# Optimization experiments

Hardware: AMD Instinct MI355X
Metric: run time of the kernel (lower is better)

The kernel has to match this reference:

```python
import jax, jax.numpy as jnp
import numpy as np

HEADS = 16
DIM_HEAD = 64
QUERY_DIM = 1024
INNER = HEADS * DIM_HEAD
SCALE = DIM_HEAD ** -0.5


def setup_inputs() -> dict:
    key = jax.random.key(0)
    ks = jax.random.split(key, 6)
    B, N, M = 2, 2048, 2048
    x = jax.random.normal(ks[0], (B, N, QUERY_DIM), dtype=jnp.float32)
    context = jax.random.normal(ks[1], (B, M, QUERY_DIM), dtype=jnp.float32)
    s = QUERY_DIM ** -0.5
    # weights stored [in, out] so y = x @ W matches torch Linear(x) with W = weight.T
    Wq = jax.random.normal(ks[2], (QUERY_DIM, INNER), dtype=jnp.float32) * s
    Wk = jax.random.normal(ks[3], (QUERY_DIM, INNER), dtype=jnp.float32) * s
    Wv = jax.random.normal(ks[4], (QUERY_DIM, INNER), dtype=jnp.float32) * s
    Wo = jax.random.normal(ks[5], (INNER, QUERY_DIM), dtype=jnp.float32) * (INNER ** -0.5)
    return {"x": x, "context": context, "Wq": Wq, "Wk": Wk, "Wv": Wv, "Wo": Wo}


def reference(x, context, Wq, Wk, Wv, Wo):
    B, N, _ = x.shape
    M = context.shape[1]
    # projections -> [b, n, h, d]
    q = (x @ Wq).reshape(B, N, HEADS, DIM_HEAD)
    k = (context @ Wk).reshape(B, M, HEADS, DIM_HEAD)
    v = (context @ Wv).reshape(B, M, HEADS, DIM_HEAD)
    sim = jnp.einsum('bihd,bjhd->bhij', q, k) * SCALE  # [b, h, n, m]
    attn = jax.nn.softmax(sim, axis=-1)
    out = jnp.einsum('bhij,bjhd->bihd', attn, v)  # [b, n, h, d]
    out = out.reshape(B, N, INNER)
    return out @ Wo
```

## Files before the change

### kernel.cpp

```cpp
#include <hip/hip_runtime.h>
#include <hip/hip_bf16.h>


typedef __attribute__((ext_vector_type(8))) __bf16    bf16x8;
typedef __attribute__((ext_vector_type(4))) __bf16    bf16x4;
typedef __attribute__((ext_vector_type(4))) float     f32x4;

#define B_    2
#define H_    16
#define N_    2048
#define M_    2048
#define D_    64
#define QD_   1024

#define QSCALE 0.18033688011112042f

__device__ __forceinline__ void gld16(const __bf16* g, __bf16* l) {
    __builtin_amdgcn_global_load_lds(
        (const __attribute__((address_space(1))) unsigned int*)(g),
        (__attribute__((address_space(3))) unsigned int*)(l), 16, 0, 0);
}

__global__ __launch_bounds__(256) void prep(const float* __restrict__ x,
                                            const float* __restrict__ ctx,
                                            const float* __restrict__ w0,
                                            const float* __restrict__ w1,
                                            const float* __restrict__ w2,
                                            const float* __restrict__ w3,
                                            __bf16* __restrict__ xb,
                                            __bf16* __restrict__ cb,
                                            __bf16* __restrict__ t0,
                                            __bf16* __restrict__ t1,
                                            __bf16* __restrict__ t2,
                                            __bf16* __restrict__ t3) {
    __shared__ float tile[64][65];
    const int z = blockIdx.z;
    if (z < 2) {
        const float* src = z ? ctx : x;
        __bf16*      dst = z ? cb  : xb;
        const size_t base = (size_t)(blockIdx.y * 16 + blockIdx.x) * 16384;
#pragma unroll
        for (int p = 0; p < 16; ++p) {
            size_t i = base + p * 1024 + threadIdx.x * 4;
            float4 v = *reinterpret_cast<const float4*>(src + i);
            bf16x4 o;
            o.x = (__bf16)v.x; o.y = (__bf16)v.y; o.z = (__bf16)v.z; o.w = (__bf16)v.w;
            *reinterpret_cast<bf16x4*>(dst + i) = o;
        }
        return;
    }
    const int w = z - 2;
    const float* in = (w == 0) ? w0 : (w == 1) ? w1 : (w == 2) ? w2 : w3;
    __bf16*     out = (w == 0) ? t0 : (w == 1) ? t1 : (w == 2) ? t2 : t3;
    const int i0 = blockIdx.x * 64;
    const int o0 = blockIdx.y * 64;
    const int t  = threadIdx.x;
    const int r  = t >> 4;
    const int c4 = (t & 15) * 4;
#pragma unroll
    for (int p = 0; p < 4; ++p) {
        int row = p * 16 + r;
        float4 v = *reinterpret_cast<const float4*>(in + (size_t)(i0 + row) * QD_ + o0 + c4);
        tile[row][c4 + 0] = v.x; tile[row][c4 + 1] = v.y;
        tile[row][c4 + 2] = v.z; tile[row][c4 + 3] = v.w;
    }
    __syncthreads();
#pragma unroll
    for (int p = 0; p < 4; ++p) {
        int orow = p * 16 + r;
        bf16x4 o;
        o.x = (__bf16)tile[c4 + 0][orow];
        o.y = (__bf16)tile[c4 + 1][orow];
        o.z = (__bf16)tile[c4 + 2][orow];
        o.w = (__bf16)tile[c4 + 3][orow];
        *reinterpret_cast<bf16x4*>(out + (size_t)(o0 + orow) * QD_ + i0 + c4) = o;
    }
}

__global__ __launch_bounds__(256) void gemm_qkv(const __bf16* __restrict__ xb,
                                                const __bf16* __restrict__ cb,
                                                const __bf16* __restrict__ Wtq,
                                                const __bf16* __restrict__ Wtk,
                                                const __bf16* __restrict__ Wtv,
                                                __bf16* __restrict__ Qb,
                                                __bf16* __restrict__ Kb,
                                                __bf16* __restrict__ Vt) {
    __shared__ __align__(16) __bf16 POOL[17408];
    __bf16* const Al0 = POOL;
    __bf16* const Al1 = POOL + 4096;
    __bf16* const Bl0 = POOL + 8192;
    __bf16* const Bl1 = POOL + 12288;

    const int z = blockIdx.z;
    const __bf16* A_  = (z == 0) ? xb : cb;
    const __bf16* Bt_ = (z == 0) ? Wtq : (z == 1) ? Wtk : Wtv;

    const int tid  = threadIdx.x;
    const int wid  = tid >> 6;
    const int lane = tid & 63;
    const int l15  = lane & 15;
    const int lg   = lane >> 4;
    const int wr   = wid >> 1;
    const int wc   = wid & 1;
    const int rowBase = blockIdx.x * 128;
    const int colBase = blockIdx.y * 128;
    const int srow = wid * 32 + (lane >> 2);
    const int sg   = ((lane & 3) ^ ((srow >> 1) & 3)) * 8;
    const __bf16* Ag  = A_  + (size_t)(rowBase + srow) * QD_ + sg;
    const __bf16* Ag2 = Ag  + (size_t)16 * QD_;
    const __bf16* Bg  = Bt_ + (size_t)(colBase + srow) * QD_ + sg;
    const __bf16* Bg2 = Bg  + (size_t)16 * QD_;
    const int sOff  = (wid * 32) * 32;
    const int sOff2 = sOff + 16 * 32;
    int aoff[4], boff[4];
#pragma unroll
    for (int m = 0; m < 4; ++m) {
        int ra = wr * 64 + m * 16 + l15;
        int rb = wc * 64 + m * 16 + l15;
        aoff[m] = ra * 32 + ((lg ^ ((ra >> 1) & 3)) * 8);
        boff[m] = rb * 32 + ((lg ^ ((rb >> 1) & 3)) * 8);
    }
    f32x4 acc[4][4] = {};

#define GCOMPUTE(AL, BL)                                                                       \
    {                                                                                          \
        bf16x8 a[4], b[4];                                                                     \
        _Pragma("unroll")                                                                      \
        for (int m = 0; m < 4; ++m)                                                            \
            a[m] = *reinterpret_cast<const bf16x8*>(&(AL)[aoff[m]]);                           \
        _Pragma("unroll")                                                                      \
        for (int n = 0; n < 4; ++n)                                                            \
            b[n] = *reinterpret_cast<const bf16x8*>(&(BL)[boff[n]]);                           \
        _Pragma("unroll")                                                                      \
        for (int m = 0; m < 4; ++m)                                                            \
            _Pragma("unroll")                                                                  \
            for (int n = 0; n < 4; ++n)                                                        \
                acc[m][n] = __builtin_amdgcn_mfma_f32_16x16x32_bf16(a[m], b[n], acc[m][n], 0, 0, 0); \
    }

    gld16(Ag,  Al0 + sOff);
    gld16(Ag2, Al0 + sOff2);
    gld16(Bg,  Bl0 + sOff);
    gld16(Bg2, Bl0 + sOff2);
    __syncthreads();
    for (int t = 0; t < 32; t += 2) {
        if (t + 1 < 32) {
            int kn = (t + 1) * 32;
            gld16(Ag + kn,  Al1 + sOff);
            gld16(Ag2 + kn, Al1 + sOff2);
            gld16(Bg + kn,  Bl1 + sOff);
            gld16(Bg2 + kn, Bl1 + sOff2);
        }
        GCOMPUTE(Al0, Bl0)
        __syncthreads();
        if (t + 2 < 32) {
            int kn = (t + 2) * 32;
            gld16(Ag + kn,  Al0 + sOff);
            gld16(Ag2 + kn, Al0 + sOff2);
            gld16(Bg + kn,  Bl0 + sOff);
            gld16(Bg2 + kn, Bl0 + sOff2);
        }
        GCOMPUTE(Al1, Bl1)
        __syncthreads();
    }
#undef GCOMPUTE

#pragma unroll
    for (int m = 0; m < 4; ++m)
#pragma unroll
        for (int n = 0; n < 4; ++n)
#pragma unroll
            for (int r = 0; r < 4; ++r) {
                float v = acc[m][n][r];
                if (z == 0) v *= QSCALE;
                int rl = wr * 64 + m * 16 + lg * 4 + r;
                int cl = wc * 64 + n * 16 + l15;
                if (z == 2) POOL[cl * 136 + rl] = (__bf16)v;
                else        POOL[rl * 136 + cl] = (__bf16)v;
            }
    __syncthreads();

    const int prow0 = tid >> 4;
    const int pcol  = (tid & 15) * 8;
#pragma unroll
    for (int s = 0; s < 8; ++s) {
        int row = s * 16 + prow0;
        bf16x8 vv = *reinterpret_cast<const bf16x8*>(&POOL[row * 136 + pcol]);
        if (z == 2) {
            int cc = colBase + row, rr = rowBase + pcol;
            int b_ = rr >> 11, mm = rr & 2047, hh = cc >> 6, dd = cc & 63;
            *reinterpret_cast<bf16x8*>(&Vt[((size_t)(b_ * H_ + hh) * D_ + dd) * M_ + mm]) = vv;
        } else {
            int rr = rowBase + row, cc = colBase + pcol;
            int b_ = rr >> 11, nn = rr & 2047, hh = cc >> 6, dd = cc & 63;
            __bf16* dst = (z == 0) ? Qb : Kb;
            *reinterpret_cast<bf16x8*>(&dst[((size_t)(b_ * H_ + hh) * N_ + nn) * D_ + dd]) = vv;
        }
    }
}

__global__ __launch_bounds__(256) void gemm_out(const __bf16* __restrict__ AO,
                                                const __bf16* __restrict__ Wto,
                                                float* __restrict__ out) {
    __shared__ __align__(16) __bf16 POOL[17408];
    __bf16* const Al0 = POOL;
    __bf16* const Al1 = POOL + 4096;
    __bf16* const Bl0 = POOL + 8192;
    __bf16* const Bl1 = POOL + 10240;

    const int tid  = threadIdx.x;
    const int wid  = tid >> 6;
    const int lane = tid & 63;
    const int l15  = lane & 15;
    const int lg   = lane >> 4;
    const int wr   = wid >> 1;
    const int wc   = wid & 1;
    const int rowBase = blockIdx.x * 128;
    const int colBase = blockIdx.y * 64;
    const int srowA = wid * 32 + (lane >> 2);
    const int srowB = wid * 16 + (lane >> 2);
    const int sgA   = ((lane & 3) ^ ((srowA >> 1) & 3)) * 8;
    const int sgB   = ((lane & 3) ^ ((srowB >> 1) & 3)) * 8;
    const __bf16* Ag  = AO  + (size_t)(rowBase + srowA) * QD_ + sgA;
    const __bf16* Ag2 = Ag  + (size_t)16 * QD_;
    const __bf16* Bg  = Wto + (size_t)(colBase + srowB) * QD_ + sgB;
    const int sOffA  = (wid * 32) * 32;
    const int sOffA2 = sOffA + 16 * 32;
    const int sOffB  = (wid * 16) * 32;
    int aoff[4], boff[2];
#pragma unroll
    for (int m = 0; m < 4; ++m) {
        int ra = wr * 64 + m * 16 + l15;
        aoff[m] = ra * 32 + ((lg ^ ((ra >> 1) & 3)) * 8);
    }
#pragma unroll
    for (int n = 0; n < 2; ++n) {
        int rb = wc * 32 + n * 16 + l15;
        boff[n] = rb * 32 + ((lg ^ ((rb >> 1) & 3)) * 8);
    }
    f32x4 acc[4][2] = {};

#define GCOMPUTE2(AL, BL)                                                                      \
    {                                                                                          \
        bf16x8 a[4], b[2];                                                                     \
        _Pragma("unroll")                                                                      \
        for (int m = 0; m < 4; ++m)                                                            \
            a[m] = *reinterpret_cast<const bf16x8*>(&(AL)[aoff[m]]);                           \
        _Pragma("unroll")                                                                      \
        for (int n = 0; n < 2; ++n)                                                            \
            b[n] = *reinterpret_cast<const bf16x8*>(&(BL)[boff[n]]);                           \
        _Pragma("unroll")                                                                      \
        for (int m = 0; m < 4; ++m)                                                            \
            _Pragma("unroll")                                                                  \
            for (int n = 0; n < 2; ++n)                                                        \
                acc[m][n] = __builtin_amdgcn_mfma_f32_16x16x32_bf16(a[m], b[n], acc[m][n], 0, 0, 0); \
    }

    gld16(Ag,  Al0 + sOffA);
    gld16(Ag2, Al0 + sOffA2);
    gld16(Bg,  Bl0 + sOffB);
    __syncthreads();
    for (int t = 0; t < 32; t += 2) {
        if (t + 1 < 32) {
            int kn = (t + 1) * 32;
            gld16(Ag + kn,  Al1 + sOffA);
            gld16(Ag2 + kn, Al1 + sOffA2);
            gld16(Bg + kn,  Bl1 + sOffB);
        }
        GCOMPUTE2(Al0, Bl0)
        __syncthreads();
        if (t + 2 < 32) {
            int kn = (t + 2) * 32;
            gld16(Ag + kn,  Al0 + sOffA);
            gld16(Ag2 + kn, Al0 + sOffA2);
            gld16(Bg + kn,  Bl0 + sOffB);
        }
        GCOMPUTE2(Al1, Bl1)
        __syncthreads();
    }
#undef GCOMPUTE2

    float* FP = reinterpret_cast<float*>(POOL);
#pragma unroll
    for (int m = 0; m < 4; ++m)
#pragma unroll
        for (int n = 0; n < 2; ++n)
#pragma unroll
            for (int r = 0; r < 4; ++r) {
                int rl = wr * 64 + m * 16 + lg * 4 + r;
                int cl = wc * 32 + n * 16 + l15;
                FP[rl * 68 + cl] = acc[m][n][r];
            }
    __syncthreads();
    const int prow0 = tid >> 4;
    const int pcol4 = (tid & 15) * 4;
#pragma unroll
    for (int s = 0; s < 8; ++s) {
        int row = s * 16 + prow0;
        float4 vv = *reinterpret_cast<const float4*>(&FP[row * 68 + pcol4]);
        *reinterpret_cast<float4*>(&out[(size_t)(rowBase + row) * QD_ + colBase + pcol4]) = vv;
    }
}

__global__ __launch_bounds__(512, 4) void attn_kernel(const __bf16* __restrict__ Q,
                                                      const __bf16* __restrict__ K,
                                                      const __bf16* __restrict__ Vt,
                                                      __bf16* __restrict__ AO) {
    __shared__ __align__(16) __bf16 POOL[32768];

    const int logical = (blockIdx.x & 7) * 64 + (blockIdx.x >> 3);
    const int qt   = logical & 15;
    const int bh   = logical >> 4;
    const int b    = bh >> 4;
    const int h    = bh & 15;
    const int wid  = threadIdx.x >> 6;
    const int grp  = wid >> 2;
    const int wl   = wid & 3;
    const int lane = threadIdx.x & 63;
    const int l15  = lane & 15;
    const int lg   = lane >> 4;
    const int qbase = qt * 128 + wl * 32;
    const int kv0   = grp << 10;

    const __bf16* Qp = Q  + ((size_t)bh * N_ + qbase) * D_;
    const __bf16* Kp = K  + (size_t)bh * M_ * D_;
    const __bf16* Vp = Vt + (size_t)bh * D_ * M_;

    const int srow = (wl << 4) + (lane >> 3);
    const int scol = (lane & 7) << 3;
    const int sk0  = (lane >> 3) & 3;
    const int sk1  = sk0 | 4;
    const int sv   = lane >> 3;
    const int kc0  = scol ^ (sk0 << 3);
    const int kc1  = scol ^ (sk1 << 3);
    const int vc   = scol ^ (sv  << 3);

    __bf16* const K0 = POOL + (grp * 2 + 0) * 4096;
    __bf16* const K1 = POOL + (grp * 2 + 1) * 4096;
    __bf16* const V0 = POOL + 16384 + (grp * 2 + 0) * 4096;
    __bf16* const V1 = POOL + 16384 + (grp * 2 + 1) * 4096;
    __bf16* const k0d = K0 + wl * 1024;
    __bf16* const k1d = K1 + wl * 1024;
    __bf16* const v0d = V0 + wl * 1024;
    __bf16* const v1d = V1 + wl * 1024;

#define STAGE(KD, VD, KV)                                                      \
    gld16(Kp + (size_t)((KV) + srow)     * D_ + kc0, (KD));                    \
    gld16(Kp + (size_t)((KV) + srow + 8) * D_ + kc1, (KD) + 512);              \
    gld16(Vp + (size_t)(srow)     * M_ + (KV) + vc,  (VD));                    \
    gld16(Vp + (size_t)(srow + 8) * M_ + (KV) + vc,  (VD) + 512);

    const int rm0 = ((l15 >> 2) * 8) + (l15 & 3);
    const int skq = (l15 & 3) | (((l15 >> 2) & 1) << 2);
    const int svq = l15 & 7;
    const int ak00 = rm0 * 64 + (( 0 + lg * 8) ^ (skq << 3));
    const int ak01 = rm0 * 64 + ((32 + lg * 8) ^ (skq << 3));
    const int ak10 = ak00 + 256;
    const int ak11 = ak01 + 256;
    const int av0 = l15 * 64 + (( 0 + lg * 8) ^ (svq << 3));
    const int av1 = l15 * 64 + ((32 + lg * 8) ^ (svq << 3));

    bf16x8 qf00 = *reinterpret_cast<const bf16x8*>(Qp + (size_t)(l15)      * D_ +      lg * 8);
    bf16x8 qf01 = *reinterpret_cast<const bf16x8*>(Qp + (size_t)(l15)      * D_ + 32 + lg * 8);
    bf16x8 qf10 = *reinterpret_cast<const bf16x8*>(Qp + (size_t)(16 + l15) * D_ +      lg * 8);
    bf16x8 qf11 = *reinterpret_cast<const bf16x8*>(Qp + (size_t)(16 + l15) * D_ + 32 + lg * 8);

    bf16x8 onesf;
#pragma unroll
    for (int j = 0; j < 8; ++j) onesf[j] = (__bf16)1.0f;

    f32x4 o00 = {}, o01 = {}, o10 = {}, o11 = {};
    f32x4 o20 = {}, o21 = {}, o30 = {}, o31 = {};
    f32x4 ors0 = {}, ors1 = {};

#define COMPUTE(KB, VB, KOFF, AV)                                                               \
    {                                                                                           \
        bf16x8 k00 = *reinterpret_cast<const bf16x8*>((KB) + ak00 + (KOFF));                    \
        bf16x8 k01 = *reinterpret_cast<const bf16x8*>((KB) + ak01 + (KOFF));                    \
        bf16x8 k10 = *reinterpret_cast<const bf16x8*>((KB) + ak10 + (KOFF));                    \
        bf16x8 k11 = *reinterpret_cast<const bf16x8*>((KB) + ak11 + (KOFF));                    \
        bf16x8 v0  = *reinterpret_cast<const bf16x8*>((VB) + (AV));                             \
        bf16x8 v1  = *reinterpret_cast<const bf16x8*>((VB) + (AV) + 1024);                      \
        bf16x8 v2  = *reinterpret_cast<const bf16x8*>((VB) + (AV) + 2048);                      \
        bf16x8 v3  = *reinterpret_cast<const bf16x8*>((VB) + (AV) + 3072);                      \
        f32x4 s00 = {}, s01 = {}, s10 = {}, s11 = {};                                           \
        __builtin_amdgcn_s_setprio(1);                                                          \
        s00 = __builtin_amdgcn_mfma_f32_16x16x32_bf16(k00, qf00, s00, 0, 0, 0);                 \
        s00 = __builtin_amdgcn_mfma_f32_16x16x32_bf16(k01, qf01, s00, 0, 0, 0);                 \
        s01 = __builtin_amdgcn_mfma_f32_16x16x32_bf16(k00, qf10, s01, 0, 0, 0);                 \
        s01 = __builtin_amdgcn_mfma_f32_16x16x32_bf16(k01, qf11, s01, 0, 0, 0);                 \
        s10 = __builtin_amdgcn_mfma_f32_16x16x32_bf16(k10, qf00, s10, 0, 0, 0);                 \
        s10 = __builtin_amdgcn_mfma_f32_16x16x32_bf16(k11, qf01, s10, 0, 0, 0);                 \
        s11 = __builtin_amdgcn_mfma_f32_16x16x32_bf16(k10, qf10, s11, 0, 0, 0);                 \
        s11 = __builtin_amdgcn_mfma_f32_16x16x32_bf16(k11, qf11, s11, 0, 0, 0);                 \
        __builtin_amdgcn_s_setprio(0);                                                          \
        bf16x8 pf0, pf1;                                                                        \
        pf0[0] = (__bf16)__builtin_amdgcn_exp2f(s00[0]);                                        \
        pf0[1] = (__bf16)__builtin_amdgcn_exp2f(s00[1]);                                        \
        pf0[2] = (__bf16)__builtin_amdgcn_exp2f(s00[2]);                                        \
        pf0[3] = (__bf16)__builtin_amdgcn_exp2f(s00[3]);                                        \
        pf0[4] = (__bf16)__builtin_amdgcn_exp2f(s10[0]);                                        \
        pf0[5] = (__bf16)__builtin_amdgcn_exp2f(s10[1]);                                        \
        pf0[6] = (__bf16)__builtin_amdgcn_exp2f(s10[2]);                                        \
        pf0[7] = (__bf16)__builtin_amdgcn_exp2f(s10[3]);                                        \
        pf1[0] = (__bf16)__builtin_amdgcn_exp2f(s01[0]);                                        \
        pf1[1] = (__bf16)__builtin_amdgcn_exp2f(s01[1]);                                        \
        pf1[2] = (__bf16)__builtin_amdgcn_exp2f(s01[2]);                                        \
        pf1[3] = (__bf16)__builtin_amdgcn_exp2f(s01[3]);                                        \
        pf1[4] = (__bf16)__builtin_amdgcn_exp2f(s11[0]);                                        \
        pf1[5] = (__bf16)__builtin_amdgcn_exp2f(s11[1]);                                        \
        pf1[6] = (__bf16)__builtin_amdgcn_exp2f(s11[2]);                                        \
        pf1[7] = (__bf16)__builtin_amdgcn_exp2f(s11[3]);                                        \
        __builtin_amdgcn_s_setprio(1);                                                          \
        ors0 = __builtin_amdgcn_mfma_f32_16x16x32_bf16(pf0, onesf, ors0, 0, 0, 0);              \
        ors1 = __builtin_amdgcn_mfma_f32_16x16x32_bf16(pf1, onesf, ors1, 0, 0, 0);              \
        o00 = __builtin_amdgcn_mfma_f32_16x16x32_bf16(pf0, v0, o00, 0, 0, 0);                   \
        o01 = __builtin_amdgcn_mfma_f32_16x16x32_bf16(pf1, v0, o01, 0, 0, 0);                   \
        o10 = __builtin_amdgcn_mfma_f32_16x16x32_bf16(pf0, v1, o10, 0, 0, 0);                   \
        o11 = __builtin_amdgcn_mfma_f32_16x16x32_bf16(pf1, v1, o11, 0, 0, 0);                   \
        o20 = __builtin_amdgcn_mfma_f32_16x16x32_bf16(pf0, v2, o20, 0, 0, 0);                   \
        o21 = __builtin_amdgcn_mfma_f32_16x16x32_bf16(pf1, v2, o21, 0, 0, 0);                   \
        o30 = __builtin_amdgcn_mfma_f32_16x16x32_bf16(pf0, v3, o30, 0, 0, 0);                   \
        o31 = __builtin_amdgcn_mfma_f32_16x16x32_bf16(pf1, v3, o31, 0, 0, 0);                   \
        __builtin_amdgcn_s_setprio(0);                                                          \
    }

    STAGE(k0d, v0d, kv0)
    __syncthreads();

    for (int t = 0; t < 16; t += 2) {
        if (t + 1 < 16) { STAGE(k1d, v1d, kv0 + (t + 1) * 64) }
        COMPUTE(K0, V0, 0,    av0)
        COMPUTE(K0, V0, 2048, av1)
        __syncthreads();
        if (t + 2 < 16) { STAGE(k0d, v0d, kv0 + (t + 2) * 64) }
        COMPUTE(K1, V1, 0,    av0)
        COMPUTE(K1, V1, 2048, av1)
        __syncthreads();
    }
#undef STAGE
#undef COMPUTE

    float* LO = reinterpret_cast<float*>(POOL);
    float* LS = LO + 128 * 65;
    if (grp == 1) {
#pragma unroll
        for (int r = 0; r < 4; ++r) {
            int row0 = wl * 32 + lg * 4 + r;
            int row1 = row0 + 16;
            LO[row0 * 65 +  0 + l15] = o00[r];
            LO[row0 * 65 + 16 + l15] = o10[r];
            LO[row0 * 65 + 32 + l15] = o20[r];
            LO[row0 * 65 + 48 + l15] = o30[r];
            LO[row1 * 65 +  0 + l15] = o01[r];
            LO[row1 * 65 + 16 + l15] = o11[r];
            LO[row1 * 65 + 32 + l15] = o21[r];
            LO[row1 * 65 + 48 + l15] = o31[r];
            if (l15 == 0) { LS[row0] = ors0[r]; LS[row1] = ors1[r]; }
        }
    }
    __syncthreads();
    if (grp == 0) {
#pragma unroll
        for (int r = 0; r < 4; ++r) {
            int row0 = wl * 32 + lg * 4 + r;
            int row1 = row0 + 16;
            float i0 = 1.0f / (ors0[r] + LS[row0]);
            float i1 = 1.0f / (ors1[r] + LS[row1]);
            size_t g0 = ((size_t)b * N_ + qbase + lg * 4 + r) * QD_ + h * D_ + l15;
            size_t g1 = ((size_t)b * N_ + qbase + 16 + lg * 4 + r) * QD_ + h * D_ + l15;
            AO[g0 +  0] = (__bf16)((o00[r] + LO[row0 * 65 +  0 + l15]) * i0);
            AO[g0 + 16] = (__bf16)((o10[r] + LO[row0 * 65 + 16 + l15]) * i0);
            AO[g0 + 32] = (__bf16)((o20[r] + LO[row0 * 65 + 32 + l15]) * i0);
            AO[g0 + 48] = (__bf16)((o30[r] + LO[row0 * 65 + 48 + l15]) * i0);
            AO[g1 +  0] = (__bf16)((o01[r] + LO[row1 * 65 +  0 + l15]) * i1);
            AO[g1 + 16] = (__bf16)((o11[r] + LO[row1 * 65 + 16 + l15]) * i1);
            AO[g1 + 32] = (__bf16)((o21[r] + LO[row1 * 65 + 32 + l15]) * i1);
            AO[g1 + 48] = (__bf16)((o31[r] + LO[row1 * 65 + 48 + l15]) * i1);
        }
    }
}

extern "C" void kernel_launch(void* const* d_in, const int* in_sizes, int n_in,
                              void* d_out, int out_size, void* d_ws, size_t ws_size,
                              hipStream_t stream) {
    const float* x   = (const float*)d_in[0];
    const float* ctx = (const float*)d_in[1];
    const float* Wq  = (const float*)d_in[2];
    const float* Wk  = (const float*)d_in[3];
    const float* Wv  = (const float*)d_in[4];
    const float* Wo  = (const float*)d_in[5];

    char* ws = (char*)d_ws;
    __bf16* xb  = (__bf16*)(ws);
    __bf16* cb  = (__bf16*)(ws + (8u  << 20));
    __bf16* Wtq = (__bf16*)(ws + (16u << 20));
    __bf16* Wtk = (__bf16*)(ws + (18u << 20));
    __bf16* Wtv = (__bf16*)(ws + (20u << 20));
    __bf16* Wto = (__bf16*)(ws + (22u << 20));
    __bf16* Qb  = (__bf16*)(ws + (24u << 20));
    __bf16* Kb  = (__bf16*)(ws + (32u << 20));
    __bf16* Vt  = (__bf16*)(ws + (40u << 20));
    __bf16* AO  = (__bf16*)(ws + (48u << 20));

    prep<<<dim3(16, 16, 6), 256, 0, stream>>>(x, ctx, Wq, Wk, Wv, Wo,
                                              xb, cb, Wtq, Wtk, Wtv, Wto);
    gemm_qkv<<<dim3(32, 8, 3), 256, 0, stream>>>(xb, cb, Wtq, Wtk, Wtv, Qb, Kb, Vt);
    attn_kernel<<<512, 512, 0, stream>>>(Qb, Kb, Vt, AO);
    gemm_out<<<dim3(32, 16), 256, 0, stream>>>(AO, Wto, (float*)d_out);
}
```

Baseline: 105.6 us.

## Fuse K and V projections to share context tiles; use 64-wide head tiles

The QKV projection kernel now computes the K and V projections in the same block. Each context A tile loaded into LDS is reused for both Wk and Wv. Column tiles shrink to 64 (one head), so the grid becomes 32x16x2 instead of 32x8x3. The intent is to halve the A-tile global/LDS traffic for context and simplify the output indexing, at the cost of an unbalanced grid: Q blocks do half the MFMA work of KV blocks. K and V epilogues are also serialized through shared memory.

```diff
diff --git a/kernel.cpp b/kernel.cpp
--- a/kernel.cpp
+++ b/kernel.cpp
@@ -85,16 +85,15 @@
                                                 __bf16* __restrict__ Qb,
                                                 __bf16* __restrict__ Kb,
                                                 __bf16* __restrict__ Vt) {
-    __shared__ __align__(16) __bf16 POOL[17408];
-    __bf16* const Al0 = POOL;
-    __bf16* const Al1 = POOL + 4096;
-    __bf16* const Bl0 = POOL + 8192;
-    __bf16* const Bl1 = POOL + 12288;
+    __shared__ __align__(16) __bf16 POOL[16384];
+    __bf16* const Al0  = POOL;
+    __bf16* const Al1  = POOL + 4096;
+    __bf16* const B1l0 = POOL + 8192;
+    __bf16* const B1l1 = POOL + 10240;
+    __bf16* const B2l0 = POOL + 12288;
+    __bf16* const B2l1 = POOL + 14336;
 
     const int z = blockIdx.z;
-    const __bf16* A_  = (z == 0) ? xb : cb;
-    const __bf16* Bt_ = (z == 0) ? Wtq : (z == 1) ? Wtk : Wtv;
-
     const int tid  = threadIdx.x;
     const int wid  = tid >> 6;
     const int lane = tid & 63;
@@ -103,99 +102,193 @@
     const int wr   = wid >> 1;
     const int wc   = wid & 1;
     const int rowBase = blockIdx.x * 128;
-    const int colBase = blockIdx.y * 128;
-    const int srow = wid * 32 + (lane >> 2);
-    const int sg   = ((lane & 3) ^ ((srow >> 1) & 3)) * 8;
-    const __bf16* Ag  = A_  + (size_t)(rowBase + srow) * QD_ + sg;
-    const __bf16* Ag2 = Ag  + (size_t)16 * QD_;
-    const __bf16* Bg  = Bt_ + (size_t)(colBase + srow) * QD_ + sg;
-    const __bf16* Bg2 = Bg  + (size_t)16 * QD_;
-    const int sOff  = (wid * 32) * 32;
-    const int sOff2 = sOff + 16 * 32;
-    int aoff[4], boff[4];
+    const int colBase = blockIdx.y * 64;
+    const int b_  = rowBase >> 11;
+    const int tok = rowBase & 2047;
+    const int hh  = blockIdx.y;
+
+    const int srowA = wid * 32 + (lane >> 2);
+    const int srowB = wid * 16 + (lane >> 2);
+    const int sgA   = ((lane & 3) ^ ((srowA >> 1) & 3)) * 8;
+    const int sgB   = ((lane & 3) ^ ((srowB >> 1) & 3)) * 8;
+    const int sOffA  = (wid * 32) * 32;
+    const int sOffA2 = sOffA + 16 * 32;
+    const int sOffB  = (wid * 16) * 32;
+
+    int aoff[4], boff[2];
 #pragma unroll
     for (int m = 0; m < 4; ++m) {
         int ra = wr * 64 + m * 16 + l15;
-        int rb = wc * 64 + m * 16 + l15;
         aoff[m] = ra * 32 + ((lg ^ ((ra >> 1) & 3)) * 8);
-        boff[m] = rb * 32 + ((lg ^ ((rb >> 1) & 3)) * 8);
-    }
-    f32x4 acc[4][4] = {};
-
-#define GCOMPUTE(AL, BL)                                                                       \
+    }
+#pragma unroll
+    for (int n = 0; n < 2; ++n) {
+        int rb = wc * 32 + n * 16 + l15;
+        boff[n] = rb * 32 + ((lg ^ ((rb >> 1) & 3)) * 8);
+    }
+
+    const int prow  = tid >> 3;
+    const int pcol8 = (tid & 7) * 8;
+
+    if (z == 0) {
+        const __bf16* Ag  = xb  + (size_t)(rowBase + srowA) * QD_ + sgA;
+        const __bf16* Ag2 = Ag  + (size_t)16 * QD_;
+        const __bf16* Bg  = Wtq + (size_t)(colBase + srowB) * QD_ + sgB;
+        f32x4 acc[4][2] = {};
+
+#define QCOMPUTE(AL, BL)                                                                       \
+        {                                                                                      \
+            bf16x8 a[4], b[2];                                                                 \
+            _Pragma("unroll")                                                                  \
+            for (int m = 0; m < 4; ++m)                                                        \
+                a[m] = *reinterpret_cast<const bf16x8*>(&(AL)[aoff[m]]);                       \
+            _Pragma("unroll")                                                                  \
+            for (int n = 0; n < 2; ++n)                                                        \
+                b[n] = *reinterpret_cast<const bf16x8*>(&(BL)[boff[n]]);                       \
+            _Pragma("unroll")                                                                  \
+            for (int m = 0; m < 4; ++m)                                                        \
+                _Pragma("unroll")                                                              \
+                for (int n = 0; n < 2; ++n)                                                    \
+                    acc[m][n] = __builtin_amdgcn_mfma_f32_16x16x32_bf16(a[m], b[n], acc[m][n], 0, 0, 0); \
+        }
+
+        gld16(Ag,  Al0 + sOffA);
+        gld16(Ag2, Al0 + sOffA2);
+        gld16(Bg,  B1l0 + sOffB);
+        __syncthreads();
+        for (int t = 0; t < 32; t += 2) {
+            if (t + 1 < 32) {
+                int kn = (t + 1) * 32;
+                gld16(Ag + kn,  Al1 + sOffA);
+                gld16(Ag2 + kn, Al1 + sOffA2);
+                gld16(Bg + kn,  B1l1 + sOffB);
+            }
+            QCOMPUTE(Al0, B1l0)
+            __syncthreads();
+            if (t + 2 < 32) {
+                int kn = (t + 2) * 32;
+                gld16(Ag + kn,  Al0 + sOffA);
+                gld16(Ag2 + kn, Al0 + sOffA2);
+                gld16(Bg + kn,  B1l0 + sOffB);
+            }
+            QCOMPUTE(Al1, B1l1)
+            __syncthreads();
+        }
+#undef QCOMPUTE
+
+#pragma unroll
+        for (int m = 0; m < 4; ++m)
+#pragma unroll
+            for (int n = 0; n < 2; ++n)
+#pragma unroll
+                for (int r = 0; r < 4; ++r) {
+                    int rl = wr * 64 + m * 16 + lg * 4 + r;
+                    int cl = wc * 32 + n * 16 + l15;
+                    POOL[rl * 72 + cl] = (__bf16)(acc[m][n][r] * QSCALE);
+                }
+        __syncthreads();
+#pragma unroll
+        for (int s = 0; s < 4; ++s) {
+            int row = s * 32 + prow;
+            bf16x8 vv = *reinterpret_cast<const bf16x8*>(&POOL[row * 72 + pcol8]);
+            *reinterpret_cast<bf16x8*>(
+                &Qb[((size_t)(b_ * H_ + hh) * N_ + tok + row) * D_ + pcol8]) = vv;
+        }
+        return;
+    }
+
+    const __bf16* Ag  = cb  + (size_t)(rowBase + srowA) * QD_ + sgA;
+    const __bf16* Ag2 = Ag  + (size_t)16 * QD_;
+    const __bf16* B1g = Wtk + (size_t)(colBase + srowB) * QD_ + sgB;
+    const __bf16* B2g = Wtv + (size_t)(colBase + srowB) * QD_ + sgB;
+    f32x4 accK[4][2] = {}, accV[4][2] = {};
+
+#define KVCOMPUTE(AL, B1L, B2L)                                                                \
     {                                                                                          \
-        bf16x8 a[4], b[4];                                                                     \
+        bf16x8 a[4], b1[2], b2[2];                                                             \
         _Pragma("unroll")                                                                      \
         for (int m = 0; m < 4; ++m)                                                            \
             a[m] = *reinterpret_cast<const bf16x8*>(&(AL)[aoff[m]]);                           \
         _Pragma("unroll")                                                                      \
-        for (int n = 0; n < 4; ++n)                                                            \
-            b[n] = *reinterpret_cast<const bf16x8*>(&(BL)[boff[n]]);                           \
+        for (int n = 0; n < 2; ++n) {                                                          \
+            b1[n] = *reinterpret_cast<const bf16x8*>(&(B1L)[boff[n]]);                         \
+            b2[n] = *reinterpret_cast<const bf16x8*>(&(B2L)[boff[n]]);                         \
+        }                                                                                      \
         _Pragma("unroll")                                                                      \
         for (int m = 0; m < 4; ++m)                                                            \
             _Pragma("unroll")                                                                  \
-            for (int n = 0; n < 4; ++n)                                                        \
-                acc[m][n] = __builtin_amdgcn_mfma_f32_16x16x32_bf16(a[m], b[n], acc[m][n], 0, 0, 0); \
-    }
-
-    gld16(Ag,  Al0 + sOff);
-    gld16(Ag2, Al0 + sOff2);
-    gld16(Bg,  Bl0 + sOff);
-    gld16(Bg2, Bl0 + sOff2);
+            for (int n = 0; n < 2; ++n) {                                                      \
+                accK[m][n] = __builtin_amdgcn_mfma_f32_16x16x32_bf16(a[m], b1[n], accK[m][n], 0, 0, 0); \
+                accV[m][n] = __builtin_amdgcn_mfma_f32_16x16x32_bf16(a[m], b2[n], accV[m][n], 0, 0, 0); \
+            }                                                                                  \
+    }
+
+    gld16(Ag,  Al0 + sOffA);
+    gld16(Ag2, Al0 + sOffA2);
+    gld16(B1g, B1l0 + sOffB);
+    gld16(B2g, B2l0 + sOffB);
     __syncthreads();
     for (int t = 0; t < 32; t += 2) {
         if (t + 1 < 32) {
             int kn = (t + 1) * 32;
-            gld16(Ag + kn,  Al1 + sOff);
-            gld16(Ag2 + kn, Al1 + sOff2);
-            gld16(Bg + kn,  Bl1 + sOff);
-            gld16(Bg2 + kn, Bl1 + sOff2);
-        }
-        GCOMPUTE(Al0, Bl0)
+            gld16(Ag + kn,  Al1 + sOffA);
+            gld16(Ag2 + kn, Al1 + sOffA2);
+            gld16(B1g + kn, B1l1 + sOffB);
+            gld16(B2g + kn, B2l1 + sOffB);
+        }
+        KVCOMPUTE(Al0, B1l0, B2l0)
         __syncthreads();
         if (t + 2 < 32) {
             int kn = (t + 2) * 32;
-            gld16(Ag + kn,  Al0 + sOff);
-            gld16(Ag2 + kn, Al0 + sOff2);
-            gld16(Bg + kn,  Bl0 + sOff);
-            gld16(Bg2 + kn, Bl0 + sOff2);
-        }
-        GCOMPUTE(Al1, Bl1)
-        __syncthreads();
-    }
-#undef GCOMPUTE
+            gld16(Ag + kn,  Al0 + sOffA);
+            gld16(Ag2 + kn, Al0 + sOffA2);
+            gld16(B1g + kn, B1l0 + sOffB);
+            gld16(B2g + kn, B2l0 + sOffB);
+        }
+        KVCOMPUTE(Al1, B1l1, B2l1)
+        __syncthreads();
+    }
+#undef KVCOMPUTE
 
 #pragma unroll
     for (int m = 0; m < 4; ++m)
 #pragma unroll
-        for (int n = 0; n < 4; ++n)
+        for (int n = 0; n < 2; ++n)
 #pragma unroll
             for (int r = 0; r < 4; ++r) {
-                float v = acc[m][n][r];
-                if (z == 0) v *= QSCALE;
                 int rl = wr * 64 + m * 16 + lg * 4 + r;
-                int cl = wc * 64 + n * 16 + l15;
-                if (z == 2) POOL[cl * 136 + rl] = (__bf16)v;
-                else        POOL[rl * 136 + cl] = (__bf16)v;
+                int cl = wc * 32 + n * 16 + l15;
+                POOL[rl * 72 + cl] = (__bf16)accK[m][n][r];
             }
     __syncthreads();
-
-    const int prow0 = tid >> 4;
-    const int pcol  = (tid & 15) * 8;
-#pragma unroll
-    for (int s = 0; s < 8; ++s) {
-        int row = s * 16 + prow0;
-        bf16x8 vv = *reinterpret_cast<const bf16x8*>(&POOL[row * 136 + pcol]);
-        if (z == 2) {
-            int cc = colBase + row, rr = rowBase + pcol;
-            int b_ = rr >> 11, mm = rr & 2047, hh = cc >> 6, dd = cc & 63;
-            *reinterpret_cast<bf16x8*>(&Vt[((size_t)(b_ * H_ + hh) * D_ + dd) * M_ + mm]) = vv;
-        } else {
-            int rr = rowBase + row, cc = colBase + pcol;
-            int b_ = rr >> 11, nn = rr & 2047, hh = cc >> 6, dd = cc & 63;
-            __bf16* dst = (z == 0) ? Qb : Kb;
-            *reinterpret_cast<bf16x8*>(&dst[((size_t)(b_ * H_ + hh) * N_ + nn) * D_ + dd]) = vv;
-        }
+#pragma unroll
+    for (int s = 0; s < 4; ++s) {
+        int row = s * 32 + prow;
+        bf16x8 vv = *reinterpret_cast<const bf16x8*>(&POOL[row * 72 + pcol8]);
+        *reinterpret_cast<bf16x8*>(
+            &Kb[((size_t)(b_ * H_ + hh) * N_ + tok + row) * D_ + pcol8]) = vv;
+    }
+    __syncthreads();
+
+#pragma unroll
+    for (int m = 0; m < 4; ++m)
+#pragma unroll
+        for (int n = 0; n < 2; ++n)
+#pragma unroll
+            for (int r = 0; r < 4; ++r) {
+                int rl = wr * 64 + m * 16 + lg * 4 + r;
+                int cl = wc * 32 + n * 16 + l15;
+                POOL[cl * 136 + rl] = (__bf16)accV[m][n][r];
+            }
+    __syncthreads();
+    const int vrow   = tid >> 4;
+    const int vchunk = (tid & 15) * 8;
+#pragma unroll
+    for (int s = 0; s < 4; ++s) {
+        int dd = s * 16 + vrow;
+        bf16x8 vv = *reinterpret_cast<const bf16x8*>(&POOL[dd * 136 + vchunk]);
+        *reinterpret_cast<bf16x8*>(
+            &Vt[((size_t)(b_ * H_ + hh) * D_ + dd) * M_ + tok + vchunk]) = vv;
     }
 }
 
@@ -505,7 +598,7 @@
 
     prep<<<dim3(16, 16, 6), 256, 0, stream>>>(x, ctx, Wq, Wk, Wv, Wo,
                                               xb, cb, Wtq, Wtk, Wtv, Wto);
-    gemm_qkv<<<dim3(32, 8, 3), 256, 0, stream>>>(xb, cb, Wtq, Wtk, Wtv, Qb, Kb, Vt);
+    gemm_qkv<<<dim3(32, 16, 2), 256, 0, stream>>>(xb, cb, Wtq, Wtk, Wtv, Qb, Kb, Vt);
     attn_kernel<<<512, 512, 0, stream>>>(Qb, Kb, Vt, AO);
     gemm_out<<<dim3(32, 16), 256, 0, stream>>>(AO, Wto, (float*)d_out);
 }
```

Result: slower. 110.6 us (+4.7%).
